# Optimization experiments

Hardware: AMD Instinct MI355X
Metric: run time of the kernel (lower is better)

Reference implementation:

```python
import jax, jax.numpy as jnp
import numpy as np

NUM_HEADS = 8
NUM_LAYER = 4


def setup_inputs() -> dict:
    key = jax.random.key(0)
    k1, k2, k3, k4, k5, k6, k7 = jax.random.split(key, 7)
    bs, num, C = 2, 2048, 256
    H0 = (jax.random.uniform(k1, (bs, num, num)) < 0.3).astype(jnp.float32)
    vertex_feat = jax.random.normal(k2, (bs, C, num), dtype=jnp.float32)
    edge_feat = jax.random.normal(k3, (bs, C, num), dtype=jnp.float32)
    s = 1.0 / np.sqrt(C)
    # Conv1d(kernel_size=1) weights, squeezed to [C_out, C_in]
    Wq = jax.random.uniform(k4, (C, C), minval=-s, maxval=s, dtype=jnp.float32)
    bq = jax.random.uniform(k5, (C,), minval=-s, maxval=s, dtype=jnp.float32)
    Wk = jax.random.uniform(k6, (C, C), minval=-s, maxval=s, dtype=jnp.float32)
    bk = jax.random.uniform(k7, (C,), minval=-s, maxval=s, dtype=jnp.float32)
    return {"H0": H0, "vertex_feat": vertex_feat, "edge_feat": edge_feat,
            "Wq": Wq, "bq": bq, "Wk": Wk, "bk": bk, "iter": 1}


def reference(H0, vertex_feat, edge_feat, Wq, bq, Wk, bk, iter):
    bs, num, _ = H0.shape
    C = vertex_feat.shape[1]
    h = NUM_HEADS
    d = C // h
    # 1x1 Conv1d == per-position linear; reshape to heads: [bs, h, d, num]
    Q = (jnp.einsum('oc,bcn->bon', Wq, vertex_feat) + bq[None, :, None]).reshape(bs, h, d, num)
    K = (jnp.einsum('oc,bcn->bon', Wk, edge_feat) + bk[None, :, None]).reshape(bs, h, d, num)
    attn = jnp.einsum('bhco,bhci->bhoi', Q, K) / np.sqrt(d)  # [bs, h, num, num]
    # attention_mask = (1 - H0).masked_fill((1-H0).bool(), -1e9)
    m = 1.0 - H0
    m = jnp.where(m != 0, jnp.float32(-1e9), m)
    score = jax.nn.sigmoid(attn + m[:, None, :, :]).sum(axis=1) / h  # [bs, num, num]
    # top-k row thresholding (k static: iter is a python int)
    k = max(1, round(num * 0.1 * (NUM_LAYER - 1 - iter)))
    topk_vals = jax.lax.top_k(score, k)[0]           # sorted descending
    a_min = topk_vals[..., -1:]                      # row-wise k-th largest
    W = jnp.where(score >= a_min, score, jnp.float32(0.0))
    H = jnp.where(W > 0, H0, jnp.float32(0.0))
    # degree normalizations (1e-10 keeps them finite; torch isinf branch is a no-op)
    De_n_1 = (1.0 / (H.sum(axis=1) + 1e-10))[..., None]  # [bs, num, 1]
    Dv_n_1 = (1.0 / (H.sum(axis=2) + 1e-10))[..., None]  # [bs, num, 1]
    # F.normalize(W.sum(dim=1), dim=1): L2 normalize with eps=1e-12
    W_edge = W.sum(axis=1)
    W_edge = W_edge / jnp.maximum(jnp.linalg.norm(W_edge, axis=1, keepdims=True), 1e-12)
    W_edge = W_edge[..., None]  # [bs, num, 1]
    return (H, W, De_n_1, Dv_n_1, W_edge)
```

## Files before the change

### kernel.cpp

```cpp
#include <hip/hip_runtime.h>
#include <math.h>

#define NUM 2048
#define CDIM 256
#define NUM_LAYER 4

typedef _Float16 f16x8 __attribute__((ext_vector_type(8)));
typedef unsigned short u16x8 __attribute__((ext_vector_type(8)));
typedef float f32x4 __attribute__((ext_vector_type(4)));

static __device__ __forceinline__ void split_f16(float x, unsigned short& h,
                                                 unsigned short& l) {
  _Float16 hi = (_Float16)x;
  float r = x - (float)hi;
  _Float16 lo = (_Float16)r;
  h = __builtin_bit_cast(unsigned short, hi);
  l = __builtin_bit_cast(unsigned short, lo);
}

static __device__ __forceinline__ void split3_f16(float x, unsigned short& h,
                                                  unsigned short& m,
                                                  unsigned short& l) {
  float xh = (fabsf(x) >= 6.103515625e-05f) ? x : 0.0f;
  _Float16 hi = (_Float16)xh;
  float r1 = x - (float)hi;
  float r1s = r1 * 2048.0f;
  _Float16 mi = (_Float16)r1s;
  float r2s = (r1s - (float)mi) * 2048.0f;
  _Float16 lo = (_Float16)r2s;
  h = __builtin_bit_cast(unsigned short, hi);
  m = __builtin_bit_cast(unsigned short, mi);
  l = __builtin_bit_cast(unsigned short, lo);
}

__global__ __launch_bounds__(256) void proj_kernel(
    const float* __restrict__ Wq, const float* __restrict__ bq,
    const float* __restrict__ Wk, const float* __restrict__ bk,
    const float* __restrict__ vf, const float* __restrict__ ef,
    unsigned short* __restrict__ Qhi, unsigned short* __restrict__ Qlo,
    unsigned short* __restrict__ Khi, unsigned short* __restrict__ Klo)
{
  const int z = blockIdx.z;
  const int b = z >> 1, mm2 = z & 1;
  const float* __restrict__ Wmat = mm2 ? Wk : Wq;
  const float* __restrict__ bias = mm2 ? bk : bq;
  const float* __restrict__ x = (mm2 ? ef : vf) + (size_t)b * CDIM * NUM;
  unsigned short* __restrict__ ohi = mm2 ? Khi : Qhi;
  unsigned short* __restrict__ olo = mm2 ? Klo : Qlo;

  const int n0 = blockIdx.x * 64;
  const int o0 = blockIdx.y * 64;

  __shared__ unsigned short xsh[3][64][36];
  __shared__ unsigned short wsh[3][64][36];
  __shared__ float T[64][69];

  const int t = threadIdx.x, lane = t & 63, wave = t >> 6;
  const int ml = lane & 15, quad = lane >> 4;
  const int nbl = wave * 16;

  const int cp = t >> 4;
  const int nq = t & 15;
  const int orow = t >> 2;
  const int cq = (t & 3) * 8;

  f32x4 acc0[4], acc1[4], acc2[4];
  #pragma unroll
  for (int ot = 0; ot < 4; ot++) {
    acc0[ot] = (f32x4){0.f, 0.f, 0.f, 0.f};
    acc1[ot] = (f32x4){0.f, 0.f, 0.f, 0.f};
    acc2[ot] = (f32x4){0.f, 0.f, 0.f, 0.f};
  }

  for (int cc = 0; cc < CDIM; cc += 32) {
    if (cc) __syncthreads();
    {
      const float4 f4a = *(const float4*)&x[(size_t)(cc + 2*cp) * NUM + n0 + nq*4];
      const float4 f4b = *(const float4*)&x[(size_t)(cc + 2*cp + 1) * NUM + n0 + nq*4];
      const float va[4] = {f4a.x, f4a.y, f4a.z, f4a.w};
      const float vb[4] = {f4b.x, f4b.y, f4b.z, f4b.w};
      #pragma unroll
      for (int j = 0; j < 4; j++) {
        unsigned short h0, m0, l0, h1, m1, l1;
        split3_f16(va[j], h0, m0, l0);
        split3_f16(vb[j], h1, m1, l1);
        *(unsigned*)&xsh[0][nq*4 + j][2*cp] = (unsigned)h0 | ((unsigned)h1 << 16);
        *(unsigned*)&xsh[1][nq*4 + j][2*cp] = (unsigned)m0 | ((unsigned)m1 << 16);
        *(unsigned*)&xsh[2][nq*4 + j][2*cp] = (unsigned)l0 | ((unsigned)l1 << 16);
      }
    }
    {
      const float4 w0 = *(const float4*)&Wmat[(size_t)(o0 + orow) * CDIM + cc + cq];
      const float4 w1 = *(const float4*)&Wmat[(size_t)(o0 + orow) * CDIM + cc + cq + 4];
      const float wv[8] = {w0.x, w0.y, w0.z, w0.w, w1.x, w1.y, w1.z, w1.w};
      #pragma unroll
      for (int j = 0; j < 4; j++) {
        unsigned short h0, m0, l0, h1, m1, l1;
        split3_f16(wv[2*j],   h0, m0, l0);
        split3_f16(wv[2*j+1], h1, m1, l1);
        *(unsigned*)&wsh[0][orow][cq + 2*j] = (unsigned)h0 | ((unsigned)h1 << 16);
        *(unsigned*)&wsh[1][orow][cq + 2*j] = (unsigned)m0 | ((unsigned)m1 << 16);
        *(unsigned*)&wsh[2][orow][cq + 2*j] = (unsigned)l0 | ((unsigned)l1 << 16);
      }
    }
    __syncthreads();
    const f16x8 bh = *(const f16x8*)&xsh[0][nbl + ml][quad*8];
    const f16x8 bm = *(const f16x8*)&xsh[1][nbl + ml][quad*8];
    const f16x8 bl = *(const f16x8*)&xsh[2][nbl + ml][quad*8];
    #pragma unroll
    for (int ot = 0; ot < 4; ot++) {
      const f16x8 ah = *(const f16x8*)&wsh[0][ot*16 + ml][quad*8];
      const f16x8 am = *(const f16x8*)&wsh[1][ot*16 + ml][quad*8];
      const f16x8 al = *(const f16x8*)&wsh[2][ot*16 + ml][quad*8];
      acc0[ot] = __builtin_amdgcn_mfma_f32_16x16x32_f16(ah, bh, acc0[ot], 0, 0, 0);
      acc1[ot] = __builtin_amdgcn_mfma_f32_16x16x32_f16(ah, bm, acc1[ot], 0, 0, 0);
      acc1[ot] = __builtin_amdgcn_mfma_f32_16x16x32_f16(am, bh, acc1[ot], 0, 0, 0);
      acc2[ot] = __builtin_amdgcn_mfma_f32_16x16x32_f16(ah, bl, acc2[ot], 0, 0, 0);
      acc2[ot] = __builtin_amdgcn_mfma_f32_16x16x32_f16(al, bh, acc2[ot], 0, 0, 0);
      acc2[ot] = __builtin_amdgcn_mfma_f32_16x16x32_f16(am, bm, acc2[ot], 0, 0, 0);
    }
  }

  const float S1 = 4.8828125e-04f;
  const float S2 = 2.38418579101562e-07f;
  #pragma unroll
  for (int ot = 0; ot < 4; ot++)
    #pragma unroll
    for (int r = 0; r < 4; r++)
      T[nbl + ml][ot*16 + quad*4 + r] =
          acc0[ot][r] + S1 * acc1[ot][r] + S2 * acc2[ot][r];
  __syncthreads();

  const float SC = -1.4426950408889634f * 0.17677669529663687f;
  const float osc = mm2 ? 1.0f : SC;
  const int n_l = t >> 2;
  const int oc  = (t & 3) * 16;
  float xv[16];
  #pragma unroll
  for (int j = 0; j < 4; j++) {
    const float4 bj = *(const float4*)&bias[o0 + oc + j*4];
    xv[j*4+0] = (T[n_l][oc + j*4+0] + bj.x) * osc;
    xv[j*4+1] = (T[n_l][oc + j*4+1] + bj.y) * osc;
    xv[j*4+2] = (T[n_l][oc + j*4+2] + bj.z) * osc;
    xv[j*4+3] = (T[n_l][oc + j*4+3] + bj.w) * osc;
  }
  unsigned short hi[16], lo[16];
  #pragma unroll
  for (int j = 0; j < 16; j++) split_f16(xv[j], hi[j], lo[j]);
  const size_t gb = ((size_t)b * NUM + n0 + n_l) * CDIM + o0 + oc;
  *(u16x8*)&ohi[gb]   = *(u16x8*)&hi[0];
  *(u16x8*)&ohi[gb+8] = *(u16x8*)&hi[8];
  *(u16x8*)&olo[gb]   = *(u16x8*)&lo[0];
  *(u16x8*)&olo[gb+8] = *(u16x8*)&lo[8];
}

__global__ __launch_bounds__(512, 2) void score_kernel(
    const unsigned short* __restrict__ Qhi, const unsigned short* __restrict__ Qlo,
    const unsigned short* __restrict__ Khi, const unsigned short* __restrict__ Klo,
    float* __restrict__ score)
{
  const int b = blockIdx.z;
  const int i0 = blockIdx.x * 128;
  const int o0 = blockIdx.y * 128;
  const int t = threadIdx.x, lane = t & 63, wave = t >> 6;
  const int m = lane & 15, quad = lane >> 4;
  const int obl = (wave & 1) * 64;
  const int ibl = (wave >> 1) * 32;

  __shared__ unsigned short qsh[2][2][128][36];
  __shared__ unsigned short ksh[2][2][128][36];

  const int srow = t >> 2;
  const int schk = (t & 3) * 8;
  const size_t gq = ((size_t)b * NUM + o0 + srow) * CDIM + schk;
  const size_t gk = ((size_t)b * NUM + i0 + srow) * CDIM + schk;

  f32x4 ssum[4][2];
  #pragma unroll
  for (int a = 0; a < 4; a++)
    #pragma unroll
    for (int c = 0; c < 2; c++) ssum[a][c] = (f32x4){0.f, 0.f, 0.f, 0.f};

  u16x8 pq[2], pk[2];
  pq[0] = *(const u16x8*)&Qhi[gq];
  pq[1] = *(const u16x8*)&Qlo[gq];
  pk[0] = *(const u16x8*)&Khi[gk];
  pk[1] = *(const u16x8*)&Klo[gk];
  *(u16x8*)&qsh[0][0][srow][schk] = pq[0];
  *(u16x8*)&qsh[0][1][srow][schk] = pq[1];
  *(u16x8*)&ksh[0][0][srow][schk] = pk[0];
  *(u16x8*)&ksh[0][1][srow][schk] = pk[1];
  __syncthreads();
  pq[0] = *(const u16x8*)&Qhi[gq + 32];
  pq[1] = *(const u16x8*)&Qlo[gq + 32];
  pk[0] = *(const u16x8*)&Khi[gk + 32];
  pk[1] = *(const u16x8*)&Klo[gk + 32];

  for (int h = 0; h < 8; h++) {
    const int c = h & 1;
    f16x8 a[4][2], bb[2][2];
    #pragma unroll
    for (int ot = 0; ot < 4; ot++)
      #pragma unroll
      for (int cp = 0; cp < 2; cp++)
        a[ot][cp] = *(const f16x8*)&qsh[c][cp][obl + ot*16 + m][quad*8];
    #pragma unroll
    for (int it = 0; it < 2; it++)
      #pragma unroll
      for (int cp = 0; cp < 2; cp++)
        bb[it][cp] = *(const f16x8*)&ksh[c][cp][ibl + it*16 + m][quad*8];

    __builtin_amdgcn_s_setprio(1);
    #pragma unroll
    for (int it = 0; it < 2; it++) {
      #pragma unroll
      for (int ot = 0; ot < 4; ot++) {
        f32x4 cc = (f32x4){0.f, 0.f, 0.f, 0.f};
        cc = __builtin_amdgcn_mfma_f32_16x16x32_f16(a[ot][0], bb[it][0], cc, 0, 0, 0);
        cc = __builtin_amdgcn_mfma_f32_16x16x32_f16(a[ot][0], bb[it][1], cc, 0, 0, 0);
        cc = __builtin_amdgcn_mfma_f32_16x16x32_f16(a[ot][1], bb[it][0], cc, 0, 0, 0);
        #pragma unroll
        for (int r = 0; r < 4; r++)
          ssum[ot][it][r] += __builtin_amdgcn_rcpf(1.0f + __builtin_amdgcn_exp2f(cc[r]));
      }
    }
    __builtin_amdgcn_s_setprio(0);

    if (h < 7) {
      *(u16x8*)&qsh[c^1][0][srow][schk] = pq[0];
      *(u16x8*)&qsh[c^1][1][srow][schk] = pq[1];
      *(u16x8*)&ksh[c^1][0][srow][schk] = pk[0];
      *(u16x8*)&ksh[c^1][1][srow][schk] = pk[1];
      __syncthreads();
      if (h < 6) {
        const size_t co = (size_t)(h + 2) * 32;
        pq[0] = *(const u16x8*)&Qhi[gq + co];
        pq[1] = *(const u16x8*)&Qlo[gq + co];
        pk[0] = *(const u16x8*)&Khi[gk + co];
        pk[1] = *(const u16x8*)&Klo[gk + co];
      }
    }
  }

  const int ob = o0 + obl, ib = i0 + ibl;
  #pragma unroll
  for (int ot = 0; ot < 4; ot++)
    #pragma unroll
    for (int it = 0; it < 2; it++)
      #pragma unroll
      for (int r = 0; r < 4; r++) {
        const int row = ob + ot*16 + quad*4 + r;
        const int col = ib + it*16 + m;
        const size_t idx = ((size_t)b * NUM + row) * NUM + col;
        score[idx] = ssum[ot][it][r] * 0.125f;
      }
}

__global__ __launch_bounds__(256) void topk_apply_kernel(
    float* __restrict__ scoreW, const float* __restrict__ H0,
    float* __restrict__ Hout, const int* __restrict__ iterp,
    float* __restrict__ DvOut)
{
  const int wave = threadIdx.x >> 6, lane = threadIdx.x & 63;
  const int row = blockIdx.x * 4 + wave;
  __shared__ unsigned int hist_all[4][256];
  unsigned int* __restrict__ h = hist_all[wave];
  unsigned int* __restrict__ srow = (unsigned int*)scoreW + (size_t)row * NUM;
  const float* __restrict__ h0row = H0 + (size_t)row * NUM;
  float* __restrict__ Hrow = Hout + (size_t)row * NUM;

  uint4 v[8];
  #pragma unroll
  for (int q = 0; q < 8; q++) {
    const uint4 s4 = ((const uint4*)srow)[lane + 64*q];
    const float4 m4 = ((const float4*)h0row)[lane + 64*q];
    v[q].x = (m4.x != 0.0f) ? s4.x : 0u;
    v[q].y = (m4.y != 0.0f) ? s4.y : 0u;
    v[q].z = (m4.z != 0.0f) ? s4.z : 0u;
    v[q].w = (m4.w != 0.0f) ? s4.w : 0u;
  }

  const int it = iterp[0];
  int k = (int)((double)NUM * 0.1 * (double)(NUM_LAYER - 1 - it) + 0.5);
  if (k < 1) k = 1;
  if (k > NUM) k = NUM;

  unsigned int prefix = 0;
  unsigned int rem = (unsigned int)k;

  for (int pass = 3; pass >= 0; pass--) {
    const int shift = pass * 8;
    const unsigned int pmask = (pass == 3) ? 0u : (0xFFFFFFFFu << (shift + 8));
    *(uint4*)&h[lane*4] = make_uint4(0u, 0u, 0u, 0u);
    __threadfence_block();
    unsigned int zc = 0;
    #pragma unroll
    for (int q = 0; q < 8; q++) {
      const unsigned int vv[4] = {v[q].x, v[q].y, v[q].z, v[q].w};
      #pragma unroll
      for (int e = 0; e < 4; e++) {
        unsigned int val = vv[e];
        if ((val & pmask) == prefix) {
          unsigned int bin = (val >> shift) & 255u;
          if (bin) atomicAdd(&h[bin], 1u);
          else zc++;
        }
      }
    }
    #pragma unroll
    for (int off = 32; off > 0; off >>= 1) zc += __shfl_down(zc, off, 64);
    if (lane == 0) h[0] = zc;
    __threadfence_block();
    const uint4 T = *(const uint4*)&h[lane*4];
    unsigned int s3 = T.w;
    unsigned int s2 = T.z + s3;
    unsigned int s1 = T.y + s2;
    unsigned int s0 = T.x + s1;
    unsigned int tot = s0;
    #pragma unroll
    for (int off = 1; off < 64; off <<= 1) {
      unsigned int y = __shfl_down(tot, off, 64);
      if (lane + off < 64) tot += y;
    }
    const unsigned int ac = tot - s0;
    const unsigned int cum[4]   = {s0 + ac, s1 + ac, s2 + ac, s3 + ac};
    const unsigned int above[4] = {s1 + ac, s2 + ac, s3 + ac, ac};
    int fq = -1;
    #pragma unroll
    for (int q = 0; q < 4; q++)
      if (cum[q] >= rem && above[q] < rem) fq = q;
    const unsigned long long mask = __ballot(fq >= 0);
    const int src = (int)(__ffsll((long long)mask) - 1);
    const unsigned int selbin = (fq >= 0) ? (unsigned int)(lane*4 + fq) : 0u;
    const unsigned int nrem   = (fq >= 0) ? (rem - above[fq]) : 0u;
    const unsigned int sel = (unsigned int)__shfl((int)selbin, src, 64);
    rem = (unsigned int)__shfl((int)nrem, src, 64);
    prefix |= (sel << shift);
  }

  const unsigned int amin = prefix;
  float cnt = 0.0f;
  #pragma unroll
  for (int q = 0; q < 8; q++) {
    unsigned int w0 = (v[q].x >= amin) ? v[q].x : 0u;
    unsigned int w1 = (v[q].y >= amin) ? v[q].y : 0u;
    unsigned int w2 = (v[q].z >= amin) ? v[q].z : 0u;
    unsigned int w3 = (v[q].w >= amin) ? v[q].w : 0u;
    float h0 = (w0 != 0u) ? 1.0f : 0.0f;
    float h1 = (w1 != 0u) ? 1.0f : 0.0f;
    float h2 = (w2 != 0u) ? 1.0f : 0.0f;
    float h3 = (w3 != 0u) ? 1.0f : 0.0f;
    cnt += h0 + h1 + h2 + h3;
    ((uint4*)srow)[lane + 64*q] = make_uint4(w0, w1, w2, w3);
    ((float4*)Hrow)[lane + 64*q] = make_float4(h0, h1, h2, h3);
  }
  #pragma unroll
  for (int off = 32; off > 0; off >>= 1) cnt += __shfl_down(cnt, off, 64);
  if (lane == 0) DvOut[row] = 1.0f / (cnt + 1e-10f);
}

__global__ __launch_bounds__(256) void colsum_kernel(
    const float* __restrict__ Wmat,
    float* __restrict__ colH, float* __restrict__ colW)
{
  const int b = blockIdx.z;
  const int i = (blockIdx.x * 256 + threadIdx.x) * 4;
  const int o0 = blockIdx.y * 64;
  float sh0 = 0.f, sh1 = 0.f, sh2 = 0.f, sh3 = 0.f;
  float sw0 = 0.f, sw1 = 0.f, sw2 = 0.f, sw3 = 0.f;
  for (int o = 0; o < 64; o++) {
    const float4 w = *(const float4*)&Wmat[((size_t)b * NUM + o0 + o) * NUM + i];
    sw0 += w.x; sw1 += w.y; sw2 += w.z; sw3 += w.w;
    sh0 += (w.x > 0.0f) ? 1.0f : 0.0f;
    sh1 += (w.y > 0.0f) ? 1.0f : 0.0f;
    sh2 += (w.z > 0.0f) ? 1.0f : 0.0f;
    sh3 += (w.w > 0.0f) ? 1.0f : 0.0f;
  }
  atomicAdd(&colH[b * NUM + i + 0], sh0);
  atomicAdd(&colH[b * NUM + i + 1], sh1);
  atomicAdd(&colH[b * NUM + i + 2], sh2);
  atomicAdd(&colH[b * NUM + i + 3], sh3);
  atomicAdd(&colW[b * NUM + i + 0], sw0);
  atomicAdd(&colW[b * NUM + i + 1], sw1);
  atomicAdd(&colW[b * NUM + i + 2], sw2);
  atomicAdd(&colW[b * NUM + i + 3], sw3);
}

__global__ __launch_bounds__(1024) void finalize_kernel(
    const float* __restrict__ colH, const float* __restrict__ colW,
    float* __restrict__ De, float* __restrict__ We)
{
  const int b = blockIdx.x;
  const int t = threadIdx.x;
  float cw[2];
  float sq = 0.0f;
  #pragma unroll
  for (int j = 0; j < 2; j++) {
    int i = t + 1024*j;
    float ch = colH[b * NUM + i];
    De[b * NUM + i] = 1.0f / (ch + 1e-10f);
    cw[j] = colW[b * NUM + i];
    sq += cw[j] * cw[j];
  }
  for (int off = 32; off > 0; off >>= 1) sq += __shfl_down(sq, off, 64);
  __shared__ float red[16];
  __shared__ float s_nrm;
  if ((t & 63) == 0) red[t >> 6] = sq;
  __syncthreads();
  if (t == 0) {
    float tot = 0.0f;
    for (int i2 = 0; i2 < 16; i2++) tot += red[i2];
    s_nrm = fmaxf(sqrtf(tot), 1e-12f);
  }
  __syncthreads();
  #pragma unroll
  for (int j = 0; j < 2; j++)
    We[b * NUM + t + 1024*j] = cw[j] / s_nrm;
}

extern "C" void kernel_launch(void* const* d_in, const int* in_sizes, int n_in,
                              void* d_out, int out_size, void* d_ws, size_t ws_size,
                              hipStream_t stream) {
  const float* H0 = (const float*)d_in[0];
  const float* vf = (const float*)d_in[1];
  const float* ef = (const float*)d_in[2];
  const float* Wq = (const float*)d_in[3];
  const float* bq = (const float*)d_in[4];
  const float* Wk = (const float*)d_in[5];
  const float* bk = (const float*)d_in[6];
  const int* iter = (const int*)d_in[7];

  float* out = (float*)d_out;
  const size_t nH = (size_t)2 * NUM * NUM;
  float* Hout  = out;
  float* Wout  = out + nH;
  float* DeOut = out + 2 * nH;
  float* DvOut = DeOut + 2 * NUM;
  float* WeOut = DvOut + 2 * NUM;

  float* colH = (float*)d_ws;
  float* colW = colH + 2 * NUM;

  const size_t nC = (size_t)2 * NUM * CDIM;
  unsigned short* base = (unsigned short*)Hout;
  unsigned short* Qhi = base;
  unsigned short* Qlo = base + nC;
  unsigned short* Khi = base + 2 * nC;
  unsigned short* Klo = base + 3 * nC;

  hipMemsetAsync(d_ws, 0, (size_t)2 * 2 * NUM * sizeof(float), stream);

  proj_kernel<<<dim3(NUM/64, CDIM/64, 4), 256, 0, stream>>>(
      Wq, bq, Wk, bk, vf, ef, Qhi, Qlo, Khi, Klo);
  score_kernel<<<dim3(NUM/128, NUM/128, 2), 512, 0, stream>>>(
      Qhi, Qlo, Khi, Klo, Wout);
  topk_apply_kernel<<<dim3(NUM/2), 256, 0, stream>>>(Wout, H0, Hout, iter, DvOut);
  colsum_kernel<<<dim3(NUM/1024, NUM/64, 2), 256, 0, stream>>>(Wout, colH, colW);
  finalize_kernel<<<dim3(2), 1024, 0, stream>>>(colH, colW, DeOut, WeOut);
}
```

Before: 183.2 us.

## Swap MFMA operand roles for vectorized score stores, remap blocks, split colsum finer

The score kernel now feeds K tiles as the MFMA A operand and Q tiles as B, so each lane's four accumulator values lie along a row and can be written as one float4 instead of four scattered scalar stores. Block indices are also remapped so that neighbouring workgroups are interleaved across tile groups and batches, which may change cache locality and spread work across XCDs. The colsum kernel cuts rows per block from 64 to 16 to launch more blocks, at the cost of four times as many atomics.

Measured after the change: 199.1 us. 1.09x slower.

```diff
diff --git a/kernel.cpp b/kernel.cpp
--- a/kernel.cpp
+++ b/kernel.cpp
@@ -159,13 +159,18 @@
     const unsigned short* __restrict__ Khi, const unsigned short* __restrict__ Klo,
     float* __restrict__ score)
 {
-  const int b = blockIdx.z;
-  const int i0 = blockIdx.x * 128;
-  const int o0 = blockIdx.y * 128;
+  const int p = blockIdx.x + (blockIdx.y << 4) + (blockIdx.z << 8);
+  const int g = p & 7, s = p >> 3;
+  const int bx = ((g & 1) << 3) + (s & 7);
+  const int by = (((g >> 1) & 1) << 3) + ((s >> 3) & 7);
+  const int b  = g >> 2;
+  const int i0 = bx * 128;
+  const int o0 = by * 128;
+
   const int t = threadIdx.x, lane = t & 63, wave = t >> 6;
   const int m = lane & 15, quad = lane >> 4;
-  const int obl = (wave & 1) * 64;
-  const int ibl = (wave >> 1) * 32;
+  const int obl = (wave & 3) * 32;
+  const int ibl = (wave >> 2) * 64;
 
   __shared__ unsigned short qsh[2][2][128][36];
   __shared__ unsigned short ksh[2][2][128][36];
@@ -200,28 +205,28 @@
     const int c = h & 1;
     f16x8 a[4][2], bb[2][2];
     #pragma unroll
-    for (int ot = 0; ot < 4; ot++)
+    for (int at = 0; at < 4; at++)
       #pragma unroll
       for (int cp = 0; cp < 2; cp++)
-        a[ot][cp] = *(const f16x8*)&qsh[c][cp][obl + ot*16 + m][quad*8];
-    #pragma unroll
-    for (int it = 0; it < 2; it++)
+        a[at][cp] = *(const f16x8*)&ksh[c][cp][ibl + at*16 + m][quad*8];
+    #pragma unroll
+    for (int bt = 0; bt < 2; bt++)
       #pragma unroll
       for (int cp = 0; cp < 2; cp++)
-        bb[it][cp] = *(const f16x8*)&ksh[c][cp][ibl + it*16 + m][quad*8];
+        bb[bt][cp] = *(const f16x8*)&qsh[c][cp][obl + bt*16 + m][quad*8];
 
     __builtin_amdgcn_s_setprio(1);
     #pragma unroll
-    for (int it = 0; it < 2; it++) {
-      #pragma unroll
-      for (int ot = 0; ot < 4; ot++) {
+    for (int bt = 0; bt < 2; bt++) {
+      #pragma unroll
+      for (int at = 0; at < 4; at++) {
         f32x4 cc = (f32x4){0.f, 0.f, 0.f, 0.f};
-        cc = __builtin_amdgcn_mfma_f32_16x16x32_f16(a[ot][0], bb[it][0], cc, 0, 0, 0);
-        cc = __builtin_amdgcn_mfma_f32_16x16x32_f16(a[ot][0], bb[it][1], cc, 0, 0, 0);
-        cc = __builtin_amdgcn_mfma_f32_16x16x32_f16(a[ot][1], bb[it][0], cc, 0, 0, 0);
+        cc = __builtin_amdgcn_mfma_f32_16x16x32_f16(a[at][0], bb[bt][0], cc, 0, 0, 0);
+        cc = __builtin_amdgcn_mfma_f32_16x16x32_f16(a[at][0], bb[bt][1], cc, 0, 0, 0);
+        cc = __builtin_amdgcn_mfma_f32_16x16x32_f16(a[at][1], bb[bt][0], cc, 0, 0, 0);
         #pragma unroll
         for (int r = 0; r < 4; r++)
-          ssum[ot][it][r] += __builtin_amdgcn_rcpf(1.0f + __builtin_amdgcn_exp2f(cc[r]));
+          ssum[at][bt][r] += __builtin_amdgcn_rcpf(1.0f + __builtin_amdgcn_exp2f(cc[r]));
       }
     }
     __builtin_amdgcn_s_setprio(0);
@@ -242,18 +247,19 @@
     }
   }
 
-  const int ob = o0 + obl, ib = i0 + ibl;
-  #pragma unroll
-  for (int ot = 0; ot < 4; ot++)
-    #pragma unroll
-    for (int it = 0; it < 2; it++)
-      #pragma unroll
-      for (int r = 0; r < 4; r++) {
-        const int row = ob + ot*16 + quad*4 + r;
-        const int col = ib + it*16 + m;
-        const size_t idx = ((size_t)b * NUM + row) * NUM + col;
-        score[idx] = ssum[ot][it][r] * 0.125f;
-      }
+  #pragma unroll
+  for (int bt = 0; bt < 2; bt++) {
+    const size_t rowbase = ((size_t)b * NUM + o0 + obl + bt*16 + m) * NUM;
+    #pragma unroll
+    for (int at = 0; at < 4; at++) {
+      float4 f4;
+      f4.x = ssum[at][bt][0] * 0.125f;
+      f4.y = ssum[at][bt][1] * 0.125f;
+      f4.z = ssum[at][bt][2] * 0.125f;
+      f4.w = ssum[at][bt][3] * 0.125f;
+      *(float4*)&score[rowbase + i0 + ibl + at*16 + quad*4] = f4;
+    }
+  }
 }
 
 __global__ __launch_bounds__(256) void topk_apply_kernel(
@@ -365,10 +371,10 @@
 {
   const int b = blockIdx.z;
   const int i = (blockIdx.x * 256 + threadIdx.x) * 4;
-  const int o0 = blockIdx.y * 64;
+  const int o0 = blockIdx.y * 16;
   float sh0 = 0.f, sh1 = 0.f, sh2 = 0.f, sh3 = 0.f;
   float sw0 = 0.f, sw1 = 0.f, sw2 = 0.f, sw3 = 0.f;
-  for (int o = 0; o < 64; o++) {
+  for (int o = 0; o < 16; o++) {
     const float4 w = *(const float4*)&Wmat[((size_t)b * NUM + o0 + o) * NUM + i];
     sw0 += w.x; sw1 += w.y; sw2 += w.z; sw3 += w.w;
     sh0 += (w.x > 0.0f) ? 1.0f : 0.0f;
@@ -455,6 +461,6 @@
   score_kernel<<<dim3(NUM/128, NUM/128, 2), 512, 0, stream>>>(
       Qhi, Qlo, Khi, Klo, Wout);
   topk_apply_kernel<<<dim3(NUM/2), 256, 0, stream>>>(Wout, H0, Hout, iter, DvOut);
-  colsum_kernel<<<dim3(NUM/1024, NUM/64, 2), 256, 0, stream>>>(Wout, colH, colW);
+  colsum_kernel<<<dim3(NUM/1024, NUM/16, 2), 256, 0, stream>>>(Wout, colH, colW);
   finalize_kernel<<<dim3(2), 1024, 0, stream>>>(colH, colW, DeOut, WeOut);
 }
```
